# Kernel optimization log

Hardware: AMD Instinct MI355X
Metric: run time of the kernel (lower is better)

## Reference

```python
import math
import jax, jax.numpy as jnp
import numpy as np

N, CH3, T = 64, 192, 2048

def setup_inputs() -> dict:
    key = jax.random.key(0)
    qkv = jax.random.normal(key, (N, CH3, T), dtype=jnp.float32)
    return {"qkv": qkv}

def reference(qkv):
    ch = qkv.shape[1] // 3
    q, k, v = jnp.split(qkv, 3, axis=1)  # each [b, c, t]
    scale = 1.0 / math.sqrt(math.sqrt(ch))
    # [b, t, s] score matrix (faithful to the naive implementation)
    weight = jnp.einsum('bct,bcs->bts', q * scale, k * scale)
    weight = jax.nn.softmax(weight.astype(jnp.float32), axis=-1).astype(weight.dtype)
    return jnp.einsum('bts,bcs->bct', weight, v)
```

## Files before the change

kernel.cpp:

```cpp
#include <hip/hip_runtime.h>
#include <math.h>


#define B_   64
#define CH_  64
#define T_   2048
#define TQ   128
#define SB   64
#define NIT  (T_ / SB)

typedef __attribute__((ext_vector_type(8))) short short8;
typedef __attribute__((ext_vector_type(4))) float f32x4;
typedef __attribute__((ext_vector_type(4))) unsigned short us4;
typedef __attribute__((ext_vector_type(8))) unsigned short us8;

static __device__ __forceinline__ unsigned short f2bf(float f) {
    union { float f; unsigned u; } v; v.f = f;
    unsigned r = v.u + 0x7FFFu + ((v.u >> 16) & 1u);
    return (unsigned short)(r >> 16);
}

static __device__ __forceinline__ short8 ld_contig(const unsigned short* p) {
    return *(const short8*)p;
}

static __device__ __forceinline__ short8 ld_strided(const unsigned short* p, int stride) {
    short8 r;
#pragma unroll
    for (int j = 0; j < 8; ++j) r[j] = (short)p[j * stride];
    return r;
}

static __device__ __forceinline__ void gl_lds16(const unsigned short* g, unsigned short* l) {
    __builtin_amdgcn_global_load_lds(
        (const __attribute__((address_space(1))) unsigned int*)g,
        (__attribute__((address_space(3))) unsigned int*)l, 16, 0, 0);
}

static __device__ __forceinline__ float vexp2(float x) {
#if __has_builtin(__builtin_amdgcn_exp2f)
    return __builtin_amdgcn_exp2f(x);
#else
    float r;
    asm("v_exp_f32 %0, %1\n\ts_nop 1" : "=v"(r) : "v"(x));
    return r;
#endif
}

static __device__ __forceinline__ unsigned cvtpk(float lo, float hi) {
    unsigned r;
    asm("v_cvt_pk_bf16_f32 %0, %1, %2" : "=v"(r) : "v"(lo), "v"(hi));
    return r;
}

static __device__ __forceinline__ void pl_swap(unsigned& a, unsigned& b) {
    asm("v_permlane32_swap_b32 %0, %1" : "+v"(a), "+v"(b));
    asm("v_permlane16_swap_b32 %0, %1" : "+v"(a), "+v"(b));
}

__global__ __launch_bounds__(256) void qkv_prep(const float* __restrict__ qkv,
                                                unsigned short* __restrict__ Ktg,
                                                unsigned short* __restrict__ Vbg)
{
    __shared__ float Tl[64][65];
    const int tid = threadIdx.x;
    const int b   = blockIdx.x >> 5;
    const int t0  = (blockIdx.x & 31) * 64;
    const float* Kp = qkv + (size_t)b * (3 * CH_ * T_) + (size_t)CH_ * T_;
    const float* Vp = Kp + (size_t)CH_ * T_;

    {
        const int c = tid & 63, fq = tid >> 6;
#pragma unroll
        for (int k = 0; k < 4; ++k) {
            const int tl = 16 * fq + 4 * k;
            const float4 v = *(const float4*)(Kp + (size_t)c * T_ + t0 + tl);
            Tl[c][tl] = v.x; Tl[c][tl + 1] = v.y; Tl[c][tl + 2] = v.z; Tl[c][tl + 3] = v.w;
        }
    }
    {
        const int c = tid >> 2, tq = (tid & 3) * 16;
        unsigned short* vout = Vbg + (size_t)b * CH_ * T_ + (size_t)c * T_ + t0 + tq;
        const float* vin = Vp + (size_t)c * T_ + t0 + tq;
#pragma unroll
        for (int k = 0; k < 2; ++k) {
            const float4 a  = *(const float4*)(vin + 8 * k);
            const float4 bq = *(const float4*)(vin + 8 * k + 4);
            us8 w8;
            w8[0]=f2bf(a.x);  w8[1]=f2bf(a.y);  w8[2]=f2bf(a.z);  w8[3]=f2bf(a.w);
            w8[4]=f2bf(bq.x); w8[5]=f2bf(bq.y); w8[6]=f2bf(bq.z); w8[7]=f2bf(bq.w);
            *(us8*)(vout + 8 * k) = w8;
        }
    }
    __syncthreads();
    {
        const int cb = tid & 7;
#pragma unroll
        for (int ot = 0; ot < 2; ++ot) {
            const int sl = (tid >> 3) + 32 * ot;
            us8 w8;
#pragma unroll
            for (int j = 0; j < 8; ++j) w8[j] = f2bf(Tl[8 * cb + j][sl]);
            *(us8*)(Ktg + (size_t)b * T_ * CH_ + (size_t)(t0 + sl) * 64 + 8 * cb) = w8;
        }
    }
}

__global__ __launch_bounds__(256, 4) void qkv_attn7(const float* __restrict__ qkv,
                                                    const unsigned short* __restrict__ Ktg,
                                                    const unsigned short* __restrict__ Vbg,
                                                    float* __restrict__ out)
{
    __shared__ unsigned short Ks[2][64 * 64];
    __shared__ unsigned short Vs[2][64 * 64];

    const int tid  = threadIdx.x;
    const int lane = tid & 63;
    const int wid  = tid >> 6;
    const int l15  = lane & 15;
    const int h    = lane >> 4;

    int bid = blockIdx.x;
    bid = (bid & 7) * 128 + (bid >> 3);
    const int b  = bid >> 4;
    const int t0 = (bid & 15) * TQ;
    const int tb = t0 + wid * 32;

    const float* Qp = qkv + (size_t)b * (3 * CH_ * T_);
    const unsigned short* Ktb = Ktg + (size_t)b * (T_ * CH_);
    const unsigned short* Vbb = Vbg + (size_t)b * (CH_ * T_);

    const int x0 = 8 * ((h)     ^ (l15 & 7));
    const int x1 = 8 * ((4 + h) ^ (l15 & 7));
    const int rb = l15 * 64;

    const int r0 = tid >> 3;
    const int kx = (tid & 7) ^ (r0 & 7);
    const unsigned short* ksrc0 = Ktb + (size_t)r0 * 64 + 8 * kx;
    const unsigned short* vsrc0 = Vbb + (size_t)r0 * T_ + 8 * kx;

    short8 aq[2][2];
#pragma unroll
    for (int ts = 0; ts < 2; ++ts)
#pragma unroll
        for (int ch = 0; ch < 2; ++ch) {
            short8 q;
#pragma unroll
            for (int j = 0; j < 8; ++j)
                q[j] = (short)f2bf(0.180336880f *
                        Qp[(size_t)(32 * ch + 8 * h + j) * T_ + tb + 16 * ts + l15]);
            aq[ts][ch] = q;
        }

    f32x4 o[4][2];
#pragma unroll
    for (int cs = 0; cs < 4; ++cs)
#pragma unroll
        for (int ts = 0; ts < 2; ++ts) o[cs][ts] = (f32x4){0.f, 0.f, 0.f, 0.f};
    float dsum[2] = {0.f, 0.f};
    const f32x4 zero4 = {0.f, 0.f, 0.f, 0.f};

    gl_lds16(ksrc0,                   &Ks[0][wid * 512]);
    gl_lds16(ksrc0 + 32 * 64,         &Ks[0][wid * 512 + 2048]);
    gl_lds16(vsrc0,                   &Vs[0][wid * 512]);
    gl_lds16(vsrc0 + (size_t)32 * T_, &Vs[0][wid * 512 + 2048]);

    for (int it = 0; it < NIT; ++it) {
        __syncthreads();
        const int buf = it & 1;
        if (it + 1 < NIT) {
            const int s1 = (it + 1) * SB;
            const int bo = (buf ^ 1) * 4096;
            gl_lds16(ksrc0 + (size_t)s1 * 64,        &Ks[0][bo + wid * 512]);
            gl_lds16(ksrc0 + (size_t)(s1 + 32) * 64, &Ks[0][bo + wid * 512 + 2048]);
            gl_lds16(vsrc0 + s1,                     &Vs[0][bo + wid * 512]);
            gl_lds16(vsrc0 + (size_t)32 * T_ + s1,   &Vs[0][bo + wid * 512 + 2048]);
        }
        const unsigned short* kb = &Ks[buf][0];
        const unsigned short* vb = &Vs[buf][0];

        __builtin_amdgcn_s_setprio(1);

        f32x4 w[2][4];
#pragma unroll
        for (int ss = 0; ss < 4; ++ss) {
            const short8 bk0 = ld_contig(kb + rb + ss * 1024 + x0);
            const short8 bk1 = ld_contig(kb + rb + ss * 1024 + x1);
#pragma unroll
            for (int ts = 0; ts < 2; ++ts) {
                f32x4 acc = zero4;
                acc = __builtin_amdgcn_mfma_f32_16x16x32_bf16(bk0, aq[ts][0], acc, 0, 0, 0);
                acc = __builtin_amdgcn_mfma_f32_16x16x32_bf16(bk1, aq[ts][1], acc, 0, 0, 0);
                w[ts][ss] = acc;
            }
        }

        short8 pb[2][2];
#pragma unroll
        for (int half = 0; half < 2; ++half)
#pragma unroll
            for (int ts = 0; ts < 2; ++ts) {
                float e0[4], e1[4];
#pragma unroll
                for (int r = 0; r < 4; ++r) {
                    e0[r] = vexp2(w[ts][2 * half + 0][r]);
                    e1[r] = vexp2(w[ts][2 * half + 1][r]);
                }
                dsum[ts] += ((e0[0] + e0[1]) + (e0[2] + e0[3]))
                          + ((e1[0] + e1[1]) + (e1[2] + e1[3]));
                unsigned a0 = cvtpk(e0[0], e0[1]);
                unsigned a1 = cvtpk(e0[2], e0[3]);
                unsigned b0 = cvtpk(e1[0], e1[1]);
                unsigned b1 = cvtpk(e1[2], e1[3]);
                pl_swap(a0, b0);
                pl_swap(a1, b1);
                union { short8 s8; unsigned u[4]; } u;
                u.u[0] = a0; u.u[1] = a1; u.u[2] = b0; u.u[3] = b1;
                pb[ts][half] = u.s8;
            }

#pragma unroll
        for (int cs = 0; cs < 4; ++cs) {
            const short8 av0 = ld_contig(vb + rb + cs * 1024 + x0);
            const short8 av1 = ld_contig(vb + rb + cs * 1024 + x1);
#pragma unroll
            for (int ts = 0; ts < 2; ++ts) {
                o[cs][ts] = __builtin_amdgcn_mfma_f32_16x16x32_bf16(av0, pb[ts][0], o[cs][ts], 0, 0, 0);
                o[cs][ts] = __builtin_amdgcn_mfma_f32_16x16x32_bf16(av1, pb[ts][1], o[cs][ts], 0, 0, 0);
            }
        }
        __builtin_amdgcn_s_setprio(0);
    }

    float inv[2];
#pragma unroll
    for (int ts = 0; ts < 2; ++ts) {
        float d = dsum[ts];
        d += __shfl_xor(d, 16, 64);
        d += __shfl_xor(d, 32, 64);
        inv[ts] = 1.0f / d;
    }

    float* outp = out + (size_t)b * CH_ * T_;
#pragma unroll
    for (int cs = 0; cs < 4; ++cs)
#pragma unroll
        for (int r = 0; r < 4; ++r) {
            const size_t row = (size_t)(16 * cs + 4 * h + r) * T_;
            outp[row + tb + l15]      = o[cs][0][r] * inv[0];
            outp[row + tb + 16 + l15] = o[cs][1][r] * inv[1];
        }
}

__global__ __launch_bounds__(256) void qkv_attn_fb(const float* __restrict__ qkv,
                                                   float* __restrict__ out)
{
    __shared__ unsigned short Qs[CH_][68];
    __shared__ unsigned short Ksf[CH_][68];
    __shared__ unsigned short Vsf[CH_][72];
    __shared__ unsigned short Psf[4][64][18];

    const int tid  = threadIdx.x;
    const int lane = tid & 63;
    const int wid  = tid >> 6;
    const int l15  = lane & 15;
    const int h    = lane >> 4;
    const int bidx = blockIdx.x;
    const int b    = bidx >> 5;
    const int t0   = (bidx & 31) * 64;
    const int tw   = wid * 16;

    const float* Qp = qkv + (size_t)b * (3 * CH_ * T_);
    const float* Kp = Qp + CH_ * T_;
    const float* Vp = Kp + CH_ * T_;

    const int srow = tid >> 4;
    const int scol = (tid & 15) << 2;

#pragma unroll
    for (int i = 0; i < 4; ++i) {
        const int c = srow + 16 * i;
        const float4 q = *(const float4*)(Qp + (size_t)c * T_ + t0 + scol);
        us4 w; w[0] = f2bf(q.x); w[1] = f2bf(q.y); w[2] = f2bf(q.z); w[3] = f2bf(q.w);
        *(us4*)(&Qs[c][scol]) = w;
    }
    __syncthreads();

    const short8 aq0 = ld_strided(&Qs[0 + 8 * h][tw + l15], 68);
    const short8 aq1 = ld_strided(&Qs[32 + 8 * h][tw + l15], 68);

    short8 aones;
#pragma unroll
    for (int j = 0; j < 8; ++j) aones[j] = (short)0x3F80;

    f32x4 o[4];
#pragma unroll
    for (int cs = 0; cs < 4; ++cs) o[cs] = (f32x4){0.f, 0.f, 0.f, 0.f};
    float l_run = 0.0f;
    const f32x4 zero4 = {0.f, 0.f, 0.f, 0.f};

    for (int it = 0; it < 32; ++it) {
        const int s0 = it * 64;
        __syncthreads();
#pragma unroll
        for (int i = 0; i < 4; ++i) {
            const int c = srow + 16 * i;
            const float4 kv = *(const float4*)(Kp + (size_t)c * T_ + s0 + scol);
            us4 wk; wk[0] = f2bf(kv.x); wk[1] = f2bf(kv.y); wk[2] = f2bf(kv.z); wk[3] = f2bf(kv.w);
            *(us4*)(&Ksf[c][scol]) = wk;
            const float4 vv = *(const float4*)(Vp + (size_t)c * T_ + s0 + scol);
            us4 wv; wv[0] = f2bf(vv.x); wv[1] = f2bf(vv.y); wv[2] = f2bf(vv.z); wv[3] = f2bf(vv.w);
            *(us4*)(&Vsf[c][scol]) = wv;
        }
        __syncthreads();

        f32x4 w[4];
#pragma unroll
        for (int ss = 0; ss < 4; ++ss) {
            const short8 bkl = ld_strided(&Ksf[0 + 8 * h][ss * 16 + l15], 68);
            const short8 bkh = ld_strided(&Ksf[32 + 8 * h][ss * 16 + l15], 68);
            f32x4 acc = zero4;
            acc = __builtin_amdgcn_mfma_f32_16x16x32_bf16(aq0, bkl, acc, 0, 0, 0);
            acc = __builtin_amdgcn_mfma_f32_16x16x32_bf16(aq1, bkh, acc, 0, 0, 0);
            w[ss] = acc;
        }

#pragma unroll
        for (int ss = 0; ss < 4; ++ss) {
            const float e0 = __expf(0.125f * w[ss][0]);
            const float e1 = __expf(0.125f * w[ss][1]);
            const float e2 = __expf(0.125f * w[ss][2]);
            const float e3 = __expf(0.125f * w[ss][3]);
            const unsigned p01 = (unsigned)f2bf(e0) | ((unsigned)f2bf(e1) << 16);
            const unsigned p23 = (unsigned)f2bf(e2) | ((unsigned)f2bf(e3) << 16);
            const int s = ss * 16 + l15;
            *(unsigned*)(&Psf[wid][s][4 * h]) = p01;
            *(unsigned*)(&Psf[wid][s][4 * h + 2]) = p23;
        }

        const short8 pb0 = ld_strided(&Psf[wid][0 + 8 * h][l15], 18);
        const short8 pb1 = ld_strided(&Psf[wid][32 + 8 * h][l15], 18);

        f32x4 lacc = zero4;
        lacc = __builtin_amdgcn_mfma_f32_16x16x32_bf16(aones, pb0, lacc, 0, 0, 0);
        lacc = __builtin_amdgcn_mfma_f32_16x16x32_bf16(aones, pb1, lacc, 0, 0, 0);
        l_run += lacc[0];

#pragma unroll
        for (int cs = 0; cs < 4; ++cs) {
            const short8 av0 = ld_contig(&Vsf[cs * 16 + l15][0 + 8 * h]);
            const short8 av1 = ld_contig(&Vsf[cs * 16 + l15][32 + 8 * h]);
            o[cs] = __builtin_amdgcn_mfma_f32_16x16x32_bf16(av0, pb0, o[cs], 0, 0, 0);
            o[cs] = __builtin_amdgcn_mfma_f32_16x16x32_bf16(av1, pb1, o[cs], 0, 0, 0);
        }
    }

    const float invd = 1.0f / l_run;
    float* outp = out + (size_t)b * CH_ * T_;
#pragma unroll
    for (int cs = 0; cs < 4; ++cs)
#pragma unroll
        for (int r = 0; r < 4; ++r)
            outp[(size_t)(cs * 16 + 4 * h + r) * T_ + t0 + tw + l15] = o[cs][r] * invd;
}

extern "C" void kernel_launch(void* const* d_in, const int* in_sizes, int n_in,
                              void* d_out, int out_size, void* d_ws, size_t ws_size,
                              hipStream_t stream) {
    const float* qkv = (const float*)d_in[0];
    float* outp = (float*)d_out;
    const size_t need = (size_t)2 * B_ * CH_ * T_ * sizeof(unsigned short);
    if (ws_size >= need) {
        unsigned short* Ktg = (unsigned short*)d_ws;
        unsigned short* Vbg = Ktg + (size_t)B_ * T_ * CH_;
        qkv_prep<<<dim3(B_ * 32), dim3(256), 0, stream>>>(qkv, Ktg, Vbg);
        qkv_attn7<<<dim3(B_ * (T_ / TQ)), dim3(256), 0, stream>>>(qkv, Ktg, Vbg, outp);
    } else {
        qkv_attn_fb<<<dim3(B_ * 32), dim3(256), 0, stream>>>(qkv, outp);
    }
}
```

Baseline: 96.45 us.

## Switch attention kernel to 32x32x16 bf16 MFMA tiles

```diff
diff --git a/kernel.cpp b/kernel.cpp
--- a/kernel.cpp
+++ b/kernel.cpp
@@ -11,6 +11,7 @@
 
 typedef __attribute__((ext_vector_type(8))) short short8;
 typedef __attribute__((ext_vector_type(4))) float f32x4;
+typedef __attribute__((ext_vector_type(16))) float f32x16;
 typedef __attribute__((ext_vector_type(4))) unsigned short us4;
 typedef __attribute__((ext_vector_type(8))) unsigned short us8;
 
@@ -51,6 +52,10 @@
     unsigned r;
     asm("v_cvt_pk_bf16_f32 %0, %1, %2" : "=v"(r) : "v"(lo), "v"(hi));
     return r;
+}
+
+static __device__ __forceinline__ void pl32(unsigned& a, unsigned& b) {
+    asm("v_permlane32_swap_b32 %0, %1" : "+v"(a), "+v"(b));
 }
 
 static __device__ __forceinline__ void pl_swap(unsigned& a, unsigned& b) {
@@ -106,7 +111,7 @@
     }
 }
 
-__global__ __launch_bounds__(256, 4) void qkv_attn7(const float* __restrict__ qkv,
+__global__ __launch_bounds__(256, 4) void qkv_attn8(const float* __restrict__ qkv,
                                                     const unsigned short* __restrict__ Ktg,
                                                     const unsigned short* __restrict__ Vbg,
                                                     float* __restrict__ out)
@@ -117,8 +122,8 @@
     const int tid  = threadIdx.x;
     const int lane = tid & 63;
     const int wid  = tid >> 6;
-    const int l15  = lane & 15;
-    const int h    = lane >> 4;
+    const int l31  = lane & 31;
+    const int hi   = lane >> 5;
 
     int bid = blockIdx.x;
     bid = (bid & 7) * 128 + (bid >> 3);
@@ -130,35 +135,33 @@
     const unsigned short* Ktb = Ktg + (size_t)b * (T_ * CH_);
     const unsigned short* Vbb = Vbg + (size_t)b * (CH_ * T_);
 
-    const int x0 = 8 * ((h)     ^ (l15 & 7));
-    const int x1 = 8 * ((4 + h) ^ (l15 & 7));
-    const int rb = l15 * 64;
+    const int sw7 = l31 & 7;
+    int kofs[4];
+#pragma unroll
+    for (int k = 0; k < 4; ++k) kofs[k] = 8 * ((2 * k + hi) ^ sw7);
+    const int rbase = l31 * 64;
 
     const int r0 = tid >> 3;
     const int kx = (tid & 7) ^ (r0 & 7);
     const unsigned short* ksrc0 = Ktb + (size_t)r0 * 64 + 8 * kx;
     const unsigned short* vsrc0 = Vbb + (size_t)r0 * T_ + 8 * kx;
 
-    short8 aq[2][2];
-#pragma unroll
-    for (int ts = 0; ts < 2; ++ts)
-#pragma unroll
-        for (int ch = 0; ch < 2; ++ch) {
-            short8 q;
-#pragma unroll
-            for (int j = 0; j < 8; ++j)
-                q[j] = (short)f2bf(0.180336880f *
-                        Qp[(size_t)(32 * ch + 8 * h + j) * T_ + tb + 16 * ts + l15]);
-            aq[ts][ch] = q;
-        }
-
-    f32x4 o[4][2];
-#pragma unroll
-    for (int cs = 0; cs < 4; ++cs)
-#pragma unroll
-        for (int ts = 0; ts < 2; ++ts) o[cs][ts] = (f32x4){0.f, 0.f, 0.f, 0.f};
-    float dsum[2] = {0.f, 0.f};
-    const f32x4 zero4 = {0.f, 0.f, 0.f, 0.f};
+    short8 aq[4];
+#pragma unroll
+    for (int ks = 0; ks < 4; ++ks) {
+        short8 q;
+#pragma unroll
+        for (int j = 0; j < 8; ++j)
+            q[j] = (short)f2bf(0.180336880f *
+                    Qp[(size_t)(16 * ks + 8 * hi + j) * T_ + tb + l31]);
+        aq[ks] = q;
+    }
+
+    f32x16 zero16;
+#pragma unroll
+    for (int r = 0; r < 16; ++r) zero16[r] = 0.0f;
+    f32x16 o0 = zero16, o1 = zero16;
+    float dsum = 0.0f;
 
     gl_lds16(ksrc0,                   &Ks[0][wid * 512]);
     gl_lds16(ksrc0 + 32 * 64,         &Ks[0][wid * 512 + 2048]);
@@ -181,75 +184,60 @@
 
         __builtin_amdgcn_s_setprio(1);
 
-        f32x4 w[2][4];
-#pragma unroll
-        for (int ss = 0; ss < 4; ++ss) {
-            const short8 bk0 = ld_contig(kb + rb + ss * 1024 + x0);
-            const short8 bk1 = ld_contig(kb + rb + ss * 1024 + x1);
-#pragma unroll
-            for (int ts = 0; ts < 2; ++ts) {
-                f32x4 acc = zero4;
-                acc = __builtin_amdgcn_mfma_f32_16x16x32_bf16(bk0, aq[ts][0], acc, 0, 0, 0);
-                acc = __builtin_amdgcn_mfma_f32_16x16x32_bf16(bk1, aq[ts][1], acc, 0, 0, 0);
-                w[ts][ss] = acc;
-            }
-        }
-
-        short8 pb[2][2];
-#pragma unroll
-        for (int half = 0; half < 2; ++half)
-#pragma unroll
-            for (int ts = 0; ts < 2; ++ts) {
-                float e0[4], e1[4];
-#pragma unroll
-                for (int r = 0; r < 4; ++r) {
-                    e0[r] = vexp2(w[ts][2 * half + 0][r]);
-                    e1[r] = vexp2(w[ts][2 * half + 1][r]);
-                }
-                dsum[ts] += ((e0[0] + e0[1]) + (e0[2] + e0[3]))
-                          + ((e1[0] + e1[1]) + (e1[2] + e1[3]));
-                unsigned a0 = cvtpk(e0[0], e0[1]);
-                unsigned a1 = cvtpk(e0[2], e0[3]);
-                unsigned b0 = cvtpk(e1[0], e1[1]);
-                unsigned b1 = cvtpk(e1[2], e1[3]);
-                pl_swap(a0, b0);
-                pl_swap(a1, b1);
-                union { short8 s8; unsigned u[4]; } u;
-                u.u[0] = a0; u.u[1] = a1; u.u[2] = b0; u.u[3] = b1;
-                pb[ts][half] = u.s8;
-            }
-
-#pragma unroll
-        for (int cs = 0; cs < 4; ++cs) {
-            const short8 av0 = ld_contig(vb + rb + cs * 1024 + x0);
-            const short8 av1 = ld_contig(vb + rb + cs * 1024 + x1);
-#pragma unroll
-            for (int ts = 0; ts < 2; ++ts) {
-                o[cs][ts] = __builtin_amdgcn_mfma_f32_16x16x32_bf16(av0, pb[ts][0], o[cs][ts], 0, 0, 0);
-                o[cs][ts] = __builtin_amdgcn_mfma_f32_16x16x32_bf16(av1, pb[ts][1], o[cs][ts], 0, 0, 0);
-            }
+        f32x16 w0 = zero16, w1 = zero16;
+#pragma unroll
+        for (int ks = 0; ks < 4; ++ks) {
+            const short8 k0 = ld_contig(kb + rbase + kofs[ks]);
+            const short8 k1 = ld_contig(kb + 2048 + rbase + kofs[ks]);
+            w0 = __builtin_amdgcn_mfma_f32_32x32x16_bf16(k0, aq[ks], w0, 0, 0, 0);
+            w1 = __builtin_amdgcn_mfma_f32_32x32x16_bf16(k1, aq[ks], w1, 0, 0, 0);
+        }
+
+#pragma unroll
+        for (int st = 0; st < 2; ++st) {
+            const f32x16 w = st ? w1 : w0;
+            float e[16];
+#pragma unroll
+            for (int r = 0; r < 16; ++r) e[r] = vexp2(st ? w1[r] : w0[r]);
+            dsum += (((e[0] + e[1]) + (e[2] + e[3])) + ((e[4] + e[5]) + (e[6] + e[7])))
+                  + (((e[8] + e[9]) + (e[10] + e[11])) + ((e[12] + e[13]) + (e[14] + e[15])));
+            unsigned P0 = cvtpk(e[0], e[1]);
+            unsigned P1 = cvtpk(e[2], e[3]);
+            unsigned P2 = cvtpk(e[4], e[5]);
+            unsigned P3 = cvtpk(e[6], e[7]);
+            unsigned P4 = cvtpk(e[8], e[9]);
+            unsigned P5 = cvtpk(e[10], e[11]);
+            unsigned P6 = cvtpk(e[12], e[13]);
+            unsigned P7 = cvtpk(e[14], e[15]);
+            pl32(P0, P2);
+            pl32(P1, P3);
+            pl32(P4, P6);
+            pl32(P5, P7);
+            union { short8 s8; unsigned u[4]; } pba, pbb;
+            pba.u[0] = P0; pba.u[1] = P1; pba.u[2] = P2; pba.u[3] = P3;
+            pbb.u[0] = P4; pbb.u[1] = P5; pbb.u[2] = P6; pbb.u[3] = P7;
+            const short8 va0 = ld_contig(vb + rbase + kofs[2 * st]);
+            const short8 va1 = ld_contig(vb + rbase + kofs[2 * st + 1]);
+            const short8 vb0 = ld_contig(vb + 2048 + rbase + kofs[2 * st]);
+            const short8 vb1 = ld_contig(vb + 2048 + rbase + kofs[2 * st + 1]);
+            o0 = __builtin_amdgcn_mfma_f32_32x32x16_bf16(va0, pba.s8, o0, 0, 0, 0);
+            o0 = __builtin_amdgcn_mfma_f32_32x32x16_bf16(va1, pbb.s8, o0, 0, 0, 0);
+            o1 = __builtin_amdgcn_mfma_f32_32x32x16_bf16(vb0, pba.s8, o1, 0, 0, 0);
+            o1 = __builtin_amdgcn_mfma_f32_32x32x16_bf16(vb1, pbb.s8, o1, 0, 0, 0);
         }
         __builtin_amdgcn_s_setprio(0);
     }
 
-    float inv[2];
-#pragma unroll
-    for (int ts = 0; ts < 2; ++ts) {
-        float d = dsum[ts];
-        d += __shfl_xor(d, 16, 64);
-        d += __shfl_xor(d, 32, 64);
-        inv[ts] = 1.0f / d;
-    }
+    float d = dsum + __shfl_xor(dsum, 32, 64);
+    const float inv = 1.0f / d;
 
     float* outp = out + (size_t)b * CH_ * T_;
 #pragma unroll
-    for (int cs = 0; cs < 4; ++cs)
-#pragma unroll
-        for (int r = 0; r < 4; ++r) {
-            const size_t row = (size_t)(16 * cs + 4 * h + r) * T_;
-            outp[row + tb + l15]      = o[cs][0][r] * inv[0];
-            outp[row + tb + 16 + l15] = o[cs][1][r] * inv[1];
-        }
+    for (int r = 0; r < 16; ++r) {
+        const int crow = (r & 3) + 8 * (r >> 2) + 4 * hi;
+        outp[(size_t)crow * T_ + tb + l31]        = o0[r] * inv;
+        outp[(size_t)(32 + crow) * T_ + tb + l31] = o1[r] * inv;
+    }
 }
 
 __global__ __launch_bounds__(256) void qkv_attn_fb(const float* __restrict__ qkv,
@@ -374,7 +362,7 @@
         unsigned short* Ktg = (unsigned short*)d_ws;
         unsigned short* Vbg = Ktg + (size_t)B_ * T_ * CH_;
         qkv_prep<<<dim3(B_ * 32), dim3(256), 0, stream>>>(qkv, Ktg, Vbg);
-        qkv_attn7<<<dim3(B_ * (T_ / TQ)), dim3(256), 0, stream>>>(qkv, Ktg, Vbg, outp);
+        qkv_attn8<<<dim3(B_ * (T_ / TQ)), dim3(256), 0, stream>>>(qkv, Ktg, Vbg, outp);
     } else {
         qkv_attn_fb<<<dim3(B_ * 32), dim3(256), 0, stream>>>(qkv, outp);
     }
```

New measurement: 96.76 us. Within noise of the previous version (+0.3%).
